# Optimization experiments

Measured on AMD Instinct MI355X. Metric: run time of the kernel, lower is better.

The kernel has to match this reference:

```python
import jax, jax.numpy as jnp
import numpy as np

MATCH_THRESH = 0.5
NEG_POS = 3
VAR0, VAR1 = 0.1, 0.2
THETA = 0.99
NEG_INF = -1e30


def point_form(c):
    # (cx, cy, w, h) -> (x1, y1, x2, y2)
    return jnp.concatenate([c[..., :2] - c[..., 2:] / 2, c[..., :2] + c[..., 2:] / 2], -1)


def iou(a, b):
    # a: [M,4] point form, b: [A,4] point form -> [M,A]
    lt = jnp.maximum(a[:, None, :2], b[None, :, :2])
    rb = jnp.minimum(a[:, None, 2:], b[None, :, 2:])
    wh = jnp.clip(rb - lt, 0.0)
    inter = wh[..., 0] * wh[..., 1]
    area_a = ((a[:, 2] - a[:, 0]) * (a[:, 3] - a[:, 1]))[:, None]
    area_b = ((b[:, 2] - b[:, 0]) * (b[:, 3] - b[:, 1]))[None, :]
    return inter / (area_a + area_b - inter)


def encode(matched, anc):
    # matched: [A,4] point-form matched GT boxes; anc: [A,4] center form
    g_cxcy = ((matched[:, :2] + matched[:, 2:]) * 0.5 - anc[:, :2]) / (VAR0 * anc[:, 2:])
    g_wh = jnp.log((matched[:, 2:] - matched[:, :2]) / anc[:, 2:]) / VAR1
    return jnp.concatenate([g_cxcy, g_wh], -1)


def match(gt_boxes, gt_labels, anc):
    # GuaranteedEncode: SSD bipartite+threshold matching with each GT guaranteed its best anchor
    M = gt_boxes.shape[0]
    ov = iou(gt_boxes, point_form(anc))  # [M, A]
    best_gt_ov = ov.max(0)               # [A]
    best_gt_idx = ov.argmax(0)           # [A]
    best_anchor = ov.argmax(1)           # [M]
    best_gt_ov = best_gt_ov.at[best_anchor].set(2.0)
    best_gt_idx = best_gt_idx.at[best_anchor].set(jnp.arange(M))
    conf = jnp.where(best_gt_ov < MATCH_THRESH, 0, gt_labels[best_gt_idx])
    loc = encode(gt_boxes[best_gt_idx], anc)
    return conf, loc


def decode(loc, anc):
    # apply ARM deltas to anchors; keep center form for re-matching
    cxcy = anc[:, :2] + loc[:, :2] * VAR0 * anc[:, 2:]
    wh = anc[:, 2:] * jnp.exp(loc[:, 2:] * VAR1)
    return jnp.concatenate([cxcy, wh], -1)


def smooth_l1(x):
    a = jnp.abs(x)
    return jnp.where(a < 1.0, 0.5 * a * a, a - 0.5)


def ce_from_logits(logits, labels):
    return -jnp.take_along_axis(jax.nn.log_softmax(logits, -1), labels[..., None], -1)[..., 0]


def setup_inputs():
    key = jax.random.key(0)
    B, A, C, M = 32, 16320, 21, 20
    ks = jax.random.split(key, 8)
    objectness = jax.random.normal(ks[0], (B, A, 2), jnp.float32)
    refine_loc = jax.random.normal(ks[1], (B, A, 4), jnp.float32)
    pred_conf = jax.random.normal(ks[2], (B, A, C), jnp.float32)
    pred_loc = jax.random.normal(ks[3], (B, A, 4), jnp.float32)
    a_cxcy = jax.random.uniform(ks[4], (1, A, 2), jnp.float32, 0.0, 1.0)
    a_wh = jax.random.uniform(ks[5], (1, A, 2), jnp.float32, 0.05, 0.5)
    anchors = jnp.concatenate([a_cxcy, a_wh], -1)  # center form
    g_cxcy = jax.random.uniform(ks[6], (B, M, 2), jnp.float32, 0.15, 0.85)
    g_wh = jax.random.uniform(ks[7], (B, M, 2), jnp.float32, 0.05, 0.3)
    gt_boxes = jnp.concatenate([g_cxcy - g_wh / 2, g_cxcy + g_wh / 2], -1)  # point form
    gt_labels = jax.random.randint(jax.random.fold_in(key, 9), (B, M), 1, C)
    return {"objectness": objectness, "refine_loc": refine_loc, "pred_conf": pred_conf,
            "pred_loc": pred_loc, "anchors": anchors, "gt_boxes": gt_boxes, "gt_labels": gt_labels}


def reference(objectness, refine_loc, pred_conf, pred_loc, anchors, gt_boxes, gt_labels):
    B, A, C = pred_conf.shape
    anc = anchors[0]
    # --- ARM stage: match GTs to fixed anchors ---
    tconf, tloc = jax.vmap(lambda gb, gl: match(gb, gl, anc))(gt_boxes, gt_labels)  # [B,A], [B,A,4]
    pos = tconf > 0
    arm_N = jnp.sum(pos).astype(jnp.float32)
    arm_loc_loss = jnp.sum(smooth_l1(refine_loc - tloc).sum(-1) * pos)
    arm_cls_loss = jnp.sum(ce_from_logits(objectness, pos.astype(jnp.int32)))
    # --- ODM stage: re-match against ARM-refined anchors, filtered by objectness ---
    object_mask = jax.nn.softmax(objectness, -1)[..., 0] < THETA  # [B,A]
    refined = jax.vmap(lambda l: decode(l, anc))(refine_loc)       # [B,A,4] center form
    tconf2, tloc2 = jax.vmap(match)(gt_boxes, gt_labels, refined)
    tloc2 = jax.lax.stop_gradient(tloc2)  # .detach() in the original
    pos2 = (tconf2 > 0) & object_mask
    N = jnp.sum(pos2).astype(jnp.float32)
    loc_loss = jnp.sum(smooth_l1(pred_loc - tloc2).sum(-1) * pos2)
    ce = ce_from_logits(pred_conf, tconf2)  # [B,A]
    pos_num = pos2.sum(-1)                  # [B]
    neg_num = jnp.maximum(10, jnp.minimum(pos_num * NEG_POS, A - pos_num))
    neg_losses = jnp.where(object_mask & (tconf2 == 0), ce, NEG_INF)
    sorted_neg = -jnp.sort(-neg_losses, axis=-1)  # descending: hard-negative mining
    take = (jnp.arange(A)[None, :] < neg_num[:, None]) & (sorted_neg > NEG_INF / 2)
    class_loss = jnp.sum(ce * pos2) + jnp.sum(jnp.where(take, sorted_neg, 0.0))
    class_loss = class_loss / N
    loc_loss = loc_loss / N
    arm_cls_loss = 0.04 * arm_cls_loss / arm_N
    arm_loc_loss = arm_loc_loss / arm_N
    total = class_loss + loc_loss + arm_cls_loss + arm_loc_loss
    return (total, class_loss, loc_loss, arm_cls_loss, arm_loc_loss)
```

## Files before the change

kernel.cpp:

```cpp
#include <hip/hip_runtime.h>
#include <math.h>

#define MATCH_THRESH 0.5f
#define THETA 0.99f
#define NEG_INF_F (-1e30f)


__device__ __forceinline__ float iou_pf(
    float ax1, float ay1, float ax2, float ay2,
    float bx1, float by1, float bx2, float by2) {
  float lx = fmaxf(ax1, bx1), ly = fmaxf(ay1, by1);
  float rx = fminf(ax2, bx2), ry = fminf(ay2, by2);
  float w = fmaxf(rx - lx, 0.f), h = fmaxf(ry - ly, 0.f);
  float inter = w * h;
  float aa = (ax2 - ax1) * (ay2 - ay1);
  float ab = (bx2 - bx1) * (by2 - by1);
  return inter / (aa + ab - inter);
}

__device__ __forceinline__ float sl1(float x) {
  float a = fabsf(x);
  return (a < 1.f) ? 0.5f * a * a : a - 0.5f;
}

__device__ __forceinline__ float wredf(float v) {
#pragma unroll
  for (int o = 32; o > 0; o >>= 1) v += __shfl_down(v, o, 64);
  return v;
}

__device__ __forceinline__ int wredi(int v) {
#pragma unroll
  for (int o = 32; o > 0; o >>= 1) v += __shfl_down(v, o, 64);
  return v;
}

__device__ __forceinline__ unsigned wredmaxu(unsigned v) {
#pragma unroll
  for (int o = 32; o > 0; o >>= 1) {
    unsigned ov = __shfl_down(v, o, 64);
    v = (ov > v) ? ov : v;
  }
  return v;
}

__device__ __forceinline__ unsigned long long wredmax64(unsigned long long v) {
#pragma unroll
  for (int o = 32; o > 0; o >>= 1) {
    unsigned lo = (unsigned)v, hi = (unsigned)(v >> 32);
    unsigned olo = __shfl_down(lo, o, 64);
    unsigned ohi = __shfl_down(hi, o, 64);
    unsigned long long ov = ((unsigned long long)ohi << 32) | olo;
    v = (ov > v) ? ov : v;
  }
  return v;
}

__device__ __forceinline__ unsigned fkey(float v) {
  unsigned b = __float_as_uint(v);
  return (b & 0x80000000u) ? ~b : (b | 0x80000000u);
}
__device__ __forceinline__ float keyf(unsigned u) {
  unsigned b = (u & 0x80000000u) ? (u & 0x7fffffffu) : ~u;
  return __uint_as_float(b);
}


template <int MM>
__global__ __launch_bounds__(256) void match_kernel(
    const float* __restrict__ gt_boxes,
    const float4* __restrict__ an4,
    const float4* __restrict__ rl4all,
    unsigned long long* __restrict__ ba1p,
    unsigned long long* __restrict__ ba2p,
    unsigned long long* __restrict__ anbA,
    unsigned long long* __restrict__ anbR,
    int B, int A) {
  int b = blockIdx.y;
  bool refined = (blockIdx.z == 1);
  unsigned long long* gdst = refined ? ba2p : ba1p;
  unsigned long long* anb = refined ? anbR : anbA;
  const float4* rl4 = rl4all + (size_t)b * A;

  __shared__ float sgb[MM * 4];
  if (threadIdx.x < MM * 4) sgb[threadIdx.x] = gt_boxes[(size_t)b * MM * 4 + threadIdx.x];
  __syncthreads();

  int chunk = (A + gridDim.x - 1) / gridDim.x;
  int start = blockIdx.x * chunk;
  int end = min(start + chunk, A);

  unsigned long long bk[MM];
#pragma unroll
  for (int m = 0; m < MM; m++) bk[m] = 0ull;

  for (int a = start + threadIdx.x; a < end; a += blockDim.x) {
    float4 an = an4[a];
    float cx = an.x, cy = an.y, w = an.z, h = an.w;
    if (refined) {
      float4 rl = rl4[a];
      cx += rl.x * 0.1f * w;
      cy += rl.y * 0.1f * h;
      w *= expf(rl.z * 0.2f);
      h *= expf(rl.w * 0.2f);
    }
    float x1 = cx - w * 0.5f, y1 = cy - h * 0.5f;
    float x2 = cx + w * 0.5f, y2 = cy + h * 0.5f;
    float bb = -1.f;
    int bi = 0;
    unsigned inva = (unsigned)(~(unsigned)a);
#pragma unroll
    for (int m = 0; m < MM; m++) {
      float v = iou_pf(sgb[m * 4], sgb[m * 4 + 1], sgb[m * 4 + 2], sgb[m * 4 + 3],
                       x1, y1, x2, y2);
      if (v > bb) { bb = v; bi = m; }
      unsigned long long key = ((unsigned long long)fkey(v) << 32) | inva;
      bk[m] = (key > bk[m]) ? key : bk[m];
    }
    anb[(size_t)b * A + a] = ((unsigned long long)fkey(bb) << 32) | (unsigned)bi;
  }

  bool lane0 = (threadIdx.x & 63) == 0;
#pragma unroll
  for (int m = 0; m < MM; m++) {
    unsigned long long k = wredmax64(bk[m]);
    if (lane0 && k) atomicMax(&gdst[(size_t)b * MM + m], k);
  }
}


__global__ __launch_bounds__(256) void gt_best_kernel(
    const float* __restrict__ gt_boxes, const float4* __restrict__ an4,
    const float4* __restrict__ rl4all, unsigned long long* __restrict__ ba1p,
    unsigned long long* __restrict__ ba2p, int B, int M, int A) {
  int bm = blockIdx.y;
  int b = bm / M;
  bool refined = (blockIdx.z == 1);
  unsigned long long* dst = refined ? ba2p : ba1p;
  const float4* rl4 = rl4all + (size_t)b * A;
  const float* g = gt_boxes + (size_t)bm * 4;
  float gx1 = g[0], gy1 = g[1], gx2 = g[2], gy2 = g[3];

  int chunk = (A + gridDim.x - 1) / gridDim.x;
  int start = blockIdx.x * chunk;
  int end = min(start + chunk, A);

  unsigned long long best = 0ull;
  for (int a = start + threadIdx.x; a < end; a += blockDim.x) {
    float4 an = an4[a];
    float cx = an.x, cy = an.y, w = an.z, h = an.w;
    if (refined) {
      float4 rl = rl4[a];
      cx += rl.x * 0.1f * w;
      cy += rl.y * 0.1f * h;
      w *= expf(rl.z * 0.2f);
      h *= expf(rl.w * 0.2f);
    }
    float v = iou_pf(gx1, gy1, gx2, gy2,
                     cx - w * 0.5f, cy - h * 0.5f, cx + w * 0.5f, cy + h * 0.5f);
    unsigned long long key =
        ((unsigned long long)fkey(v) << 32) | (unsigned)(~(unsigned)a);
    if (key > best) best = key;
  }
  best = wredmax64(best);
  __shared__ unsigned long long sm[4];
  int w = threadIdx.x >> 6;
  if ((threadIdx.x & 63) == 0) sm[w] = best;
  __syncthreads();
  if (threadIdx.x == 0) {
    unsigned long long m = sm[0];
    for (int i = 1; i < 4; i++) m = (sm[i] > m) ? sm[i] : m;
    atomicMax(&dst[bm], m);
  }
}


template <int CC, bool PRE>
__global__ __launch_bounds__(256) void loss_kernel(
    const float* __restrict__ gt_boxes, const int* __restrict__ gt_labels,
    const float* __restrict__ anchors, const float* __restrict__ refine_loc,
    const float* __restrict__ objectness, const float* __restrict__ pred_conf,
    const float* __restrict__ pred_loc,
    const unsigned long long* __restrict__ ba1p,
    const unsigned long long* __restrict__ ba2p,
    const unsigned long long* __restrict__ anbA,
    const unsigned long long* __restrict__ anbR,
    double* __restrict__ accB,
    int* __restrict__ armNB,
    int* __restrict__ poscnt,
    float* __restrict__ negl,
    int B, int M, int A, int C) {
  __shared__ float sgb[128];
  __shared__ int sb1[32], sb2[32], sgl[32];
  __shared__ float sf[4][4];
  __shared__ int sw[2][4];

  int b = blockIdx.y;
  int tid = threadIdx.x;
  if (tid < M) {
    sb1[tid] = (int)(~(unsigned)ba1p[(size_t)b * M + tid]);
    sb2[tid] = (int)(~(unsigned)ba2p[(size_t)b * M + tid]);
    sgl[tid] = gt_labels[(size_t)b * M + tid];
  }
  if (tid < M * 4) sgb[tid] = gt_boxes[(size_t)b * M * 4 + tid];
  __syncthreads();

  float p_arm_loc = 0.f, p_arm_cls = 0.f, p_loc = 0.f, p_cepos = 0.f;
  int p_armN = 0, p_pos2 = 0;

  int stride = gridDim.x * blockDim.x;
#pragma unroll 2
  for (int a = blockIdx.x * blockDim.x + tid; a < A; a += stride) {
    float pr[CC > 0 ? CC : 1];
    const float* pc = pred_conf + ((size_t)b * A + a) * C;
    if constexpr (CC > 0) {
#pragma unroll
      for (int c = 0; c < CC; c++) pr[c] = pc[c];
    }
    unsigned long long qa = 0, qr = 0;
    if constexpr (PRE) {
      qa = anbA[(size_t)b * A + a];
      qr = anbR[(size_t)b * A + a];
    }
    float4 an = ((const float4*)anchors)[a];
    float4 rl = ((const float4*)refine_loc)[(size_t)b * A + a];
    float2 ob = ((const float2*)objectness)[(size_t)b * A + a];

    float rcx = an.x + rl.x * 0.1f * an.z;
    float rcy = an.y + rl.y * 0.1f * an.w;
    float rw = an.z * expf(rl.z * 0.2f);
    float rh = an.w * expf(rl.w * 0.2f);

    float bestA, bestR;
    int biA, biR;
    if constexpr (PRE) {
      bestA = keyf((unsigned)(qa >> 32)); biA = (int)(unsigned)qa;
      bestR = keyf((unsigned)(qr >> 32)); biR = (int)(unsigned)qr;
    } else {
      float ax1 = an.x - an.z * 0.5f, ay1 = an.y - an.w * 0.5f;
      float ax2 = an.x + an.z * 0.5f, ay2 = an.y + an.w * 0.5f;
      float rx1 = rcx - rw * 0.5f, ry1 = rcy - rh * 0.5f;
      float rx2 = rcx + rw * 0.5f, ry2 = rcy + rh * 0.5f;
      bestA = -1.f; bestR = -1.f; biA = 0; biR = 0;
      for (int m = 0; m < M; m++) {
        float g0 = sgb[m * 4], g1 = sgb[m * 4 + 1], g2 = sgb[m * 4 + 2], g3 = sgb[m * 4 + 3];
        float vA = iou_pf(g0, g1, g2, g3, ax1, ay1, ax2, ay2);
        if (vA > bestA) { bestA = vA; biA = m; }
        float vR = iou_pf(g0, g1, g2, g3, rx1, ry1, rx2, ry2);
        if (vR > bestR) { bestR = vR; biR = m; }
      }
    }
    for (int m = 0; m < M; m++) {
      if (sb1[m] == a) { biA = m; bestA = 2.f; }
      if (sb2[m] == a) { biR = m; bestR = 2.f; }
    }
    int conf1 = (bestA < MATCH_THRESH) ? 0 : sgl[biA];
    int conf2 = (bestR < MATCH_THRESH) ? 0 : sgl[biR];
    int pos1 = conf1 > 0;

    if (pos1) {
      const float* g = sgb + biA * 4;
      float gcx = ((g[0] + g[2]) * 0.5f - an.x) / (0.1f * an.z);
      float gcy = ((g[1] + g[3]) * 0.5f - an.y) / (0.1f * an.w);
      float gw = logf((g[2] - g[0]) / an.z) / 0.2f;
      float gh = logf((g[3] - g[1]) / an.w) / 0.2f;
      p_arm_loc += sl1(rl.x - gcx) + sl1(rl.y - gcy) + sl1(rl.z - gw) + sl1(rl.w - gh);
    }
    float mx = fmaxf(ob.x, ob.y);
    float e0 = expf(ob.x - mx), e1 = expf(ob.y - mx);
    float lse = mx + logf(e0 + e1);
    p_arm_cls += lse - (pos1 ? ob.y : ob.x);
    p_armN += pos1;

    bool mask = (e0 / (e0 + e1)) < THETA;
    int pos2 = (conf2 > 0) && mask;

    float ce;
    if constexpr (CC > 0) {
      float mxc = pr[0];
#pragma unroll
      for (int c = 1; c < CC; c++) mxc = fmaxf(mxc, pr[c]);
      float s = 0.f;
#pragma unroll
      for (int c = 0; c < CC; c++) s += expf(pr[c] - mxc);
      float sel = pr[0];
#pragma unroll
      for (int c = 1; c < CC; c++) sel = (conf2 == c) ? pr[c] : sel;
      ce = mxc + logf(s) - sel;
    } else {
      float mxc = pc[0];
      float s = 1.f;
      for (int c = 1; c < C; c++) {
        float v = pc[c];
        float nm = fmaxf(mxc, v);
        s = s * expf(mxc - nm) + expf(v - nm);
        mxc = nm;
      }
      ce = mxc + logf(s) - pc[conf2];
    }

    if (pos2) {
      const float* g = sgb + biR * 4;
      float gcx = ((g[0] + g[2]) * 0.5f - rcx) / (0.1f * rw);
      float gcy = ((g[1] + g[3]) * 0.5f - rcy) / (0.1f * rh);
      float gw = logf((g[2] - g[0]) / rw) / 0.2f;
      float gh = logf((g[3] - g[1]) / rh) / 0.2f;
      float4 pl = ((const float4*)pred_loc)[(size_t)b * A + a];
      p_loc += sl1(pl.x - gcx) + sl1(pl.y - gcy) + sl1(pl.z - gw) + sl1(pl.w - gh);
      p_cepos += ce;
      p_pos2 += 1;
    }
    negl[(size_t)b * A + a] = (mask && conf2 == 0) ? fmaxf(ce, 0.f) : NEG_INF_F;
  }

  p_arm_loc = wredf(p_arm_loc); p_arm_cls = wredf(p_arm_cls);
  p_loc = wredf(p_loc); p_cepos = wredf(p_cepos);
  p_armN = wredi(p_armN); p_pos2 = wredi(p_pos2);
  int w = tid >> 6;
  if ((tid & 63) == 0) {
    sf[0][w] = p_arm_loc; sf[1][w] = p_arm_cls; sf[2][w] = p_loc; sf[3][w] = p_cepos;
    sw[0][w] = p_armN; sw[1][w] = p_pos2;
  }
  __syncthreads();
  if (tid == 0) {
    float aL = 0, aC = 0, oL = 0, oC = 0;
    int aN = 0, p2 = 0;
    for (int i = 0; i < 4; i++) {
      aL += sf[0][i]; aC += sf[1][i]; oL += sf[2][i]; oC += sf[3][i];
      aN += sw[0][i]; p2 += sw[1][i];
    }
    double* ab = accB + (size_t)b * 8;
    if (aL != 0.f) atomicAdd(&ab[0], (double)aL);
    atomicAdd(&ab[1], (double)aC);
    if (oL != 0.f) atomicAdd(&ab[2], (double)oL);
    if (oC != 0.f) atomicAdd(&ab[3], (double)oC);
    if (aN) atomicAdd(&armNB[b], aN);
    if (p2) atomicAdd(&poscnt[b], p2);
  }
}


__global__ __launch_bounds__(1024) void hardneg_kernel(
    const float* __restrict__ negl, const int* __restrict__ poscnt,
    const double* __restrict__ accB, const int* __restrict__ armNB,
    double* __restrict__ acc4, int* __restrict__ ctr,
    int B, int A, float* __restrict__ out) {
  int b = blockIdx.x;
  const float* nl = negl + (size_t)b * A;
  int t = threadIdx.x;
  unsigned key[16];
#pragma unroll
  for (int j = 0; j < 16; j++) {
    int i = j * 1024 + t;
    key[j] = (i < A) ? fkey(nl[i]) : 0u;
  }
  __shared__ int wcnt[2][16];
  __shared__ float wsum[16];
  __shared__ unsigned wmax[16];
  int w = t >> 6;
  bool lane0 = (t & 63) == 0;

  const unsigned UVALID = fkey(-5e29f);
  int cv = 0;
  unsigned mk = 0;
#pragma unroll
  for (int j = 0; j < 16; j++) {
    cv += (key[j] > UVALID) ? 1 : 0;
    mk = (key[j] > mk) ? key[j] : mk;
  }
  cv = wredi(cv);
  mk = wredmaxu(mk);
  if (lane0) { wcnt[0][w] = cv; wmax[w] = mk; }
  __syncthreads();
  int cnt_valid = 0;
  unsigned maxkey = 0;
  for (int i = 0; i < 16; i++) {
    cnt_valid += wcnt[0][i];
    maxkey = (wmax[i] > maxkey) ? wmax[i] : maxkey;
  }

  int pn = poscnt[b];
  int nn = max(10, min(pn * 3, A - pn));
  int K = min(nn, cnt_valid);

  if (K > 0) {
    unsigned lo = 0x7fffffffu;
    unsigned hi = (maxkey > lo) ? maxkey : lo;
    int par = 1;
    while (lo < hi) {
      unsigned d = hi - lo;
      unsigned mid = lo + (d >> 1) + (d & 1u);
      int c = 0;
#pragma unroll
      for (int j = 0; j < 16; j++) c += (key[j] >= mid) ? 1 : 0;
      c = wredi(c);
      if (lane0) wcnt[par][w] = c;
      __syncthreads();
      int tot = 0;
      for (int i = 0; i < 16; i++) tot += wcnt[par][i];
      par ^= 1;
      if (tot >= K) {
        lo = mid;
        if (tot == K) break;
      } else hi = mid - 1;
    }

    float kth = keyf(lo);
    float sum = 0.f;
    int c1 = 0;
#pragma unroll
    for (int j = 0; j < 16; j++)
      if (key[j] > lo) { sum += keyf(key[j]); c1++; }
    sum = wredf(sum);
    c1 = wredi(c1);
    __syncthreads();
    if (lane0) { wsum[w] = sum; wcnt[0][w] = c1; }
    __syncthreads();
    if (t == 0) {
      float S = 0.f;
      int C1 = 0;
      for (int i = 0; i < 16; i++) { S += wsum[i]; C1 += wcnt[0][i]; }
      S += (float)(K - C1) * kth;
      atomicAdd(acc4, (double)S);
    }
  }

  if (t == 0) {
    __threadfence();
    int old = atomicAdd(ctr, 1);
    if (old == B - 1) {
      __threadfence();
      double arm_loc = 0, arm_cls = 0, odm_loc = 0, ce_pos = 0;
      long long Ni = 0, aNi = 0;
      for (int bb = 0; bb < B; bb++) {
        const double* ab = accB + (size_t)bb * 8;
        arm_loc += ab[0]; arm_cls += ab[1]; odm_loc += ab[2]; ce_pos += ab[3];
        Ni += poscnt[bb]; aNi += armNB[bb];
      }
      double neg_sum = *acc4;
      double N = (double)Ni, armN = (double)aNi;
      double class_loss = (ce_pos + neg_sum) / N;
      double loc_loss = odm_loc / N;
      double acls = 0.04 * arm_cls / armN;
      double aloc = arm_loc / armN;
      out[0] = (float)(class_loss + loc_loss + acls + aloc);
      out[1] = (float)class_loss;
      out[2] = (float)loc_loss;
      out[3] = (float)acls;
      out[4] = (float)aloc;
    }
  }
}


extern "C" void kernel_launch(void* const* d_in, const int* in_sizes, int n_in,
                              void* d_out, int out_size, void* d_ws, size_t ws_size,
                              hipStream_t stream) {
  const float* objectness = (const float*)d_in[0];
  const float* refine_loc = (const float*)d_in[1];
  const float* pred_conf  = (const float*)d_in[2];
  const float* pred_loc   = (const float*)d_in[3];
  const float* anchors    = (const float*)d_in[4];
  const float* gt_boxes   = (const float*)d_in[5];
  const int*   gt_labels  = (const int*)d_in[6];

  int A = in_sizes[4] / 4;
  int B = in_sizes[0] / (A * 2);
  int C = (int)(in_sizes[2] / ((long long)B * A));
  int M = in_sizes[5] / (B * 4);

  char* ws = (char*)d_ws;
  double* acc4 = (double*)ws;
  int* poscnt = (int*)(ws + 64);
  int* armNB = (int*)(ws + 192);
  int* ctr = (int*)(ws + 320);
  double* accB = (double*)(ws + 512);
  size_t ba_off = 512 + (size_t)B * 64;
  unsigned long long* ba1p = (unsigned long long*)(ws + ba_off);
  unsigned long long* ba2p = (unsigned long long*)(ws + ba_off + (size_t)B * M * 8);
  size_t zero_end = ba_off + 2 * (size_t)B * M * 8;

  size_t anb_off = (zero_end + 255) & ~(size_t)255;
  size_t fast_negl_off = ((anb_off + 2 * (size_t)B * A * 8) + 255) & ~(size_t)255;
  size_t fast_need = fast_negl_off + (size_t)B * A * 4;
  bool fast = (C == 21) && (M == 20) && (B <= 32) && (ws_size >= fast_need);

  unsigned long long* anbA = (unsigned long long*)(ws + anb_off);
  unsigned long long* anbR = anbA + (size_t)B * A;
  size_t negl_off = fast ? fast_negl_off : ((zero_end + 255) & ~(size_t)255);
  float* negl = (float*)(ws + negl_off);

  hipMemsetAsync(d_ws, 0, zero_end, stream);

  if (fast) {
    dim3 mg(16, B, 2);
    match_kernel<20><<<mg, 256, 0, stream>>>(gt_boxes, (const float4*)anchors,
                                             (const float4*)refine_loc,
                                             ba1p, ba2p, anbA, anbR, B, A);
    dim3 grid(32, B);
    loss_kernel<21, true><<<grid, 256, 0, stream>>>(
        gt_boxes, gt_labels, anchors, refine_loc, objectness, pred_conf, pred_loc,
        ba1p, ba2p, anbA, anbR, accB, armNB, poscnt, negl, B, M, A, C);
  } else {
    dim3 gbg(4, B * M, 2);
    gt_best_kernel<<<gbg, 256, 0, stream>>>(gt_boxes, (const float4*)anchors,
                                            (const float4*)refine_loc, ba1p, ba2p, B, M, A);
    dim3 grid(16, B);
    loss_kernel<0, false><<<grid, 256, 0, stream>>>(
        gt_boxes, gt_labels, anchors, refine_loc, objectness, pred_conf, pred_loc,
        ba1p, ba2p, anbA, anbR, accB, armNB, poscnt, negl, B, M, A, C);
  }

  hardneg_kernel<<<B, 1024, 0, stream>>>(negl, poscnt, accB, armNB, acc4, ctr,
                                         B, A, (float*)d_out);
}
```

Measured before the change: 118.5 us.

## Split GT matching across two half-sets of boxes and use fast exp/log

The match kernel now splits the 20 GT boxes into two halves handled by separate blocks (grid z=4). Each thread keeps per-GT best IoU and anchor as a float plus index instead of 64-bit keys, and GT areas are precomputed in shared memory. The aim is more parallelism and fewer registers per thread, at the cost of writing and reading two per-anchor best arrays per stage, which the loss kernel merges. The loss kernel also switches to __expf/__logf intrinsics, and the slow path gains a templated C=21 variant.

```diff
diff --git a/kernel.cpp b/kernel.cpp
--- a/kernel.cpp
+++ b/kernel.cpp
@@ -18,6 +18,16 @@
   return inter / (aa + ab - inter);
 }
 
+__device__ __forceinline__ float iou_pf_area(
+    float ax1, float ay1, float ax2, float ay2, float aa,
+    float bx1, float by1, float bx2, float by2, float ab) {
+  float lx = fmaxf(ax1, bx1), ly = fmaxf(ay1, by1);
+  float rx = fminf(ax2, bx2), ry = fminf(ay2, by2);
+  float w = fmaxf(rx - lx, 0.f), h = fmaxf(ry - ly, 0.f);
+  float inter = w * h;
+  return inter / (aa + ab - inter);
+}
+
 __device__ __forceinline__ float sl1(float x) {
   float a = fabsf(x);
   return (a < 1.f) ? 0.5f * a * a : a - 0.5f;
@@ -66,38 +76,48 @@
 }
 
 
-template <int MM>
-__global__ __launch_bounds__(256) void match_kernel(
+template <int MH>
+__global__ __launch_bounds__(256) void match2_kernel(
     const float* __restrict__ gt_boxes,
     const float4* __restrict__ an4,
     const float4* __restrict__ rl4all,
     unsigned long long* __restrict__ ba1p,
     unsigned long long* __restrict__ ba2p,
-    unsigned long long* __restrict__ anbA,
-    unsigned long long* __restrict__ anbR,
+    unsigned long long* __restrict__ anbA0,
+    unsigned long long* __restrict__ anbA1,
+    unsigned long long* __restrict__ anbR0,
+    unsigned long long* __restrict__ anbR1,
     int B, int A) {
   int b = blockIdx.y;
-  bool refined = (blockIdx.z == 1);
-  unsigned long long* gdst = refined ? ba2p : ba1p;
-  unsigned long long* anb = refined ? anbR : anbA;
+  int stage = blockIdx.z >> 1;
+  int half = blockIdx.z & 1;
+  unsigned long long* gdst = stage ? ba2p : ba1p;
+  unsigned long long* anb = stage ? (half ? anbR1 : anbR0) : (half ? anbA1 : anbA0);
   const float4* rl4 = rl4all + (size_t)b * A;
-
-  __shared__ float sgb[MM * 4];
-  if (threadIdx.x < MM * 4) sgb[threadIdx.x] = gt_boxes[(size_t)b * MM * 4 + threadIdx.x];
+  int tid = threadIdx.x;
+
+  __shared__ float sgb[MH * 4];
+  __shared__ float sarea[MH];
+  if (tid < MH * 4)
+    sgb[tid] = gt_boxes[((size_t)b * 2 * MH + half * MH) * 4 + tid];
+  __syncthreads();
+  if (tid < MH)
+    sarea[tid] = (sgb[tid * 4 + 2] - sgb[tid * 4]) * (sgb[tid * 4 + 3] - sgb[tid * 4 + 1]);
   __syncthreads();
 
   int chunk = (A + gridDim.x - 1) / gridDim.x;
   int start = blockIdx.x * chunk;
   int end = min(start + chunk, A);
 
-  unsigned long long bk[MM];
-#pragma unroll
-  for (int m = 0; m < MM; m++) bk[m] = 0ull;
-
-  for (int a = start + threadIdx.x; a < end; a += blockDim.x) {
+  float bv[MH];
+  unsigned ba[MH];
+#pragma unroll
+  for (int m = 0; m < MH; m++) { bv[m] = -1.f; ba[m] = 0u; }
+
+  for (int a = start + tid; a < end; a += blockDim.x) {
     float4 an = an4[a];
     float cx = an.x, cy = an.y, w = an.z, h = an.w;
-    if (refined) {
+    if (stage) {
       float4 rl = rl4[a];
       cx += rl.x * 0.1f * w;
       cy += rl.y * 0.1f * h;
@@ -106,25 +126,26 @@
     }
     float x1 = cx - w * 0.5f, y1 = cy - h * 0.5f;
     float x2 = cx + w * 0.5f, y2 = cy + h * 0.5f;
+    float ab_area = (x2 - x1) * (y2 - y1);
     float bb = -1.f;
     int bi = 0;
-    unsigned inva = (unsigned)(~(unsigned)a);
-#pragma unroll
-    for (int m = 0; m < MM; m++) {
-      float v = iou_pf(sgb[m * 4], sgb[m * 4 + 1], sgb[m * 4 + 2], sgb[m * 4 + 3],
-                       x1, y1, x2, y2);
+#pragma unroll
+    for (int m = 0; m < MH; m++) {
+      float v = iou_pf_area(sgb[m * 4], sgb[m * 4 + 1], sgb[m * 4 + 2], sgb[m * 4 + 3],
+                            sarea[m], x1, y1, x2, y2, ab_area);
       if (v > bb) { bb = v; bi = m; }
-      unsigned long long key = ((unsigned long long)fkey(v) << 32) | inva;
-      bk[m] = (key > bk[m]) ? key : bk[m];
+      if (v > bv[m]) { bv[m] = v; ba[m] = (unsigned)a; }
     }
     anb[(size_t)b * A + a] = ((unsigned long long)fkey(bb) << 32) | (unsigned)bi;
   }
 
-  bool lane0 = (threadIdx.x & 63) == 0;
-#pragma unroll
-  for (int m = 0; m < MM; m++) {
-    unsigned long long k = wredmax64(bk[m]);
-    if (lane0 && k) atomicMax(&gdst[(size_t)b * MM + m], k);
+  bool lane0 = (tid & 63) == 0;
+#pragma unroll
+  for (int m = 0; m < MH; m++) {
+    unsigned long long k =
+        ((unsigned long long)fkey(bv[m]) << 32) | (unsigned)(~ba[m]);
+    k = wredmax64(k);
+    if (lane0) atomicMax(&gdst[(size_t)b * 2 * MH + half * MH + m], k);
   }
 }
 
@@ -183,8 +204,10 @@
     const float* __restrict__ pred_loc,
     const unsigned long long* __restrict__ ba1p,
     const unsigned long long* __restrict__ ba2p,
-    const unsigned long long* __restrict__ anbA,
-    const unsigned long long* __restrict__ anbR,
+    const unsigned long long* __restrict__ anbA0,
+    const unsigned long long* __restrict__ anbA1,
+    const unsigned long long* __restrict__ anbR0,
+    const unsigned long long* __restrict__ anbR1,
     double* __restrict__ accB,
     int* __restrict__ armNB,
     int* __restrict__ poscnt,
@@ -217,14 +240,15 @@
 #pragma unroll
       for (int c = 0; c < CC; c++) pr[c] = pc[c];
     }
-    unsigned long long qa = 0, qr = 0;
+    size_t idx = (size_t)b * A + a;
+    unsigned long long qa0 = 0, qa1 = 0, qr0 = 0, qr1 = 0;
     if constexpr (PRE) {
-      qa = anbA[(size_t)b * A + a];
-      qr = anbR[(size_t)b * A + a];
+      qa0 = anbA0[idx]; qa1 = anbA1[idx];
+      qr0 = anbR0[idx]; qr1 = anbR1[idx];
     }
     float4 an = ((const float4*)anchors)[a];
-    float4 rl = ((const float4*)refine_loc)[(size_t)b * A + a];
-    float2 ob = ((const float2*)objectness)[(size_t)b * A + a];
+    float4 rl = ((const float4*)refine_loc)[idx];
+    float2 ob = ((const float2*)objectness)[idx];
 
     float rcx = an.x + rl.x * 0.1f * an.z;
     float rcy = an.y + rl.y * 0.1f * an.w;
@@ -234,8 +258,14 @@
     float bestA, bestR;
     int biA, biR;
     if constexpr (PRE) {
-      bestA = keyf((unsigned)(qa >> 32)); biA = (int)(unsigned)qa;
-      bestR = keyf((unsigned)(qr >> 32)); biR = (int)(unsigned)qr;
+      unsigned f0 = (unsigned)(qa0 >> 32), f1 = (unsigned)(qa1 >> 32);
+      bool h1 = f1 > f0;
+      bestA = keyf(h1 ? f1 : f0);
+      biA = (int)(h1 ? ((unsigned)qa1 + 10u) : (unsigned)qa0);
+      unsigned g0 = (unsigned)(qr0 >> 32), g1 = (unsigned)(qr1 >> 32);
+      bool h1r = g1 > g0;
+      bestR = keyf(h1r ? g1 : g0);
+      biR = (int)(h1r ? ((unsigned)qr1 + 10u) : (unsigned)qr0);
     } else {
       float ax1 = an.x - an.z * 0.5f, ay1 = an.y - an.w * 0.5f;
       float ax2 = an.x + an.z * 0.5f, ay2 = an.y + an.w * 0.5f;
@@ -267,8 +297,8 @@
       p_arm_loc += sl1(rl.x - gcx) + sl1(rl.y - gcy) + sl1(rl.z - gw) + sl1(rl.w - gh);
     }
     float mx = fmaxf(ob.x, ob.y);
-    float e0 = expf(ob.x - mx), e1 = expf(ob.y - mx);
-    float lse = mx + logf(e0 + e1);
+    float e0 = __expf(ob.x - mx), e1 = __expf(ob.y - mx);
+    float lse = mx + __logf(e0 + e1);
     p_arm_cls += lse - (pos1 ? ob.y : ob.x);
     p_armN += pos1;
 
@@ -282,21 +312,21 @@
       for (int c = 1; c < CC; c++) mxc = fmaxf(mxc, pr[c]);
       float s = 0.f;
 #pragma unroll
-      for (int c = 0; c < CC; c++) s += expf(pr[c] - mxc);
+      for (int c = 0; c < CC; c++) s += __expf(pr[c] - mxc);
       float sel = pr[0];
 #pragma unroll
       for (int c = 1; c < CC; c++) sel = (conf2 == c) ? pr[c] : sel;
-      ce = mxc + logf(s) - sel;
+      ce = mxc + __logf(s) - sel;
     } else {
       float mxc = pc[0];
       float s = 1.f;
       for (int c = 1; c < C; c++) {
         float v = pc[c];
         float nm = fmaxf(mxc, v);
-        s = s * expf(mxc - nm) + expf(v - nm);
+        s = s * __expf(mxc - nm) + __expf(v - nm);
         mxc = nm;
       }
-      ce = mxc + logf(s) - pc[conf2];
+      ce = mxc + __logf(s) - pc[conf2];
     }
 
     if (pos2) {
@@ -305,12 +335,12 @@
       float gcy = ((g[1] + g[3]) * 0.5f - rcy) / (0.1f * rh);
       float gw = logf((g[2] - g[0]) / rw) / 0.2f;
       float gh = logf((g[3] - g[1]) / rh) / 0.2f;
-      float4 pl = ((const float4*)pred_loc)[(size_t)b * A + a];
+      float4 pl = ((const float4*)pred_loc)[idx];
       p_loc += sl1(pl.x - gcx) + sl1(pl.y - gcy) + sl1(pl.z - gw) + sl1(pl.w - gh);
       p_cepos += ce;
       p_pos2 += 1;
     }
-    negl[(size_t)b * A + a] = (mask && conf2 == 0) ? fmaxf(ce, 0.f) : NEG_INF_F;
+    negl[idx] = (mask && conf2 == 0) ? fmaxf(ce, 0.f) : NEG_INF_F;
   }
 
   p_arm_loc = wredf(p_arm_loc); p_arm_cls = wredf(p_arm_cls);
@@ -481,34 +511,44 @@
   size_t zero_end = ba_off + 2 * (size_t)B * M * 8;
 
   size_t anb_off = (zero_end + 255) & ~(size_t)255;
-  size_t fast_negl_off = ((anb_off + 2 * (size_t)B * A * 8) + 255) & ~(size_t)255;
+  size_t per = (size_t)B * A * 8;
+  size_t fast_negl_off = ((anb_off + 4 * per) + 255) & ~(size_t)255;
   size_t fast_need = fast_negl_off + (size_t)B * A * 4;
   bool fast = (C == 21) && (M == 20) && (B <= 32) && (ws_size >= fast_need);
 
-  unsigned long long* anbA = (unsigned long long*)(ws + anb_off);
-  unsigned long long* anbR = anbA + (size_t)B * A;
+  unsigned long long* anbA0 = (unsigned long long*)(ws + anb_off);
+  unsigned long long* anbA1 = anbA0 + (size_t)B * A;
+  unsigned long long* anbR0 = anbA1 + (size_t)B * A;
+  unsigned long long* anbR1 = anbR0 + (size_t)B * A;
   size_t negl_off = fast ? fast_negl_off : ((zero_end + 255) & ~(size_t)255);
   float* negl = (float*)(ws + negl_off);
 
   hipMemsetAsync(d_ws, 0, zero_end, stream);
 
   if (fast) {
-    dim3 mg(16, B, 2);
-    match_kernel<20><<<mg, 256, 0, stream>>>(gt_boxes, (const float4*)anchors,
-                                             (const float4*)refine_loc,
-                                             ba1p, ba2p, anbA, anbR, B, A);
+    dim3 mg(16, B, 4);
+    match2_kernel<10><<<mg, 256, 0, stream>>>(gt_boxes, (const float4*)anchors,
+                                              (const float4*)refine_loc,
+                                              ba1p, ba2p, anbA0, anbA1, anbR0, anbR1,
+                                              B, A);
     dim3 grid(32, B);
     loss_kernel<21, true><<<grid, 256, 0, stream>>>(
         gt_boxes, gt_labels, anchors, refine_loc, objectness, pred_conf, pred_loc,
-        ba1p, ba2p, anbA, anbR, accB, armNB, poscnt, negl, B, M, A, C);
+        ba1p, ba2p, anbA0, anbA1, anbR0, anbR1, accB, armNB, poscnt, negl, B, M, A, C);
   } else {
     dim3 gbg(4, B * M, 2);
     gt_best_kernel<<<gbg, 256, 0, stream>>>(gt_boxes, (const float4*)anchors,
                                             (const float4*)refine_loc, ba1p, ba2p, B, M, A);
     dim3 grid(16, B);
-    loss_kernel<0, false><<<grid, 256, 0, stream>>>(
-        gt_boxes, gt_labels, anchors, refine_loc, objectness, pred_conf, pred_loc,
-        ba1p, ba2p, anbA, anbR, accB, armNB, poscnt, negl, B, M, A, C);
+    if (C == 21) {
+      loss_kernel<21, false><<<grid, 256, 0, stream>>>(
+          gt_boxes, gt_labels, anchors, refine_loc, objectness, pred_conf, pred_loc,
+          ba1p, ba2p, anbA0, anbA1, anbR0, anbR1, accB, armNB, poscnt, negl, B, M, A, C);
+    } else {
+      loss_kernel<0, false><<<grid, 256, 0, stream>>>(
+          gt_boxes, gt_labels, anchors, refine_loc, objectness, pred_conf, pred_loc,
+          ba1p, ba2p, anbA0, anbA1, anbR0, anbR1, accB, armNB, poscnt, negl, B, M, A, C);
+    }
   }
 
   hardneg_kernel<<<B, 1024, 0, stream>>>(negl, poscnt, accB, armNB, acc4, ctr,
```

Measured after the change: 109.3 us. 1.08x faster.
